# Optimization experiments

Measured on AMD Instinct MI355X. Metric: run time of the kernel, lower is better.

The kernel has to match this reference:

```python
import jax, jax.numpy as jnp
import numpy as np

B, N, IN_DIM, HIDDEN, OUT_DIM, HEADS = 4, 2048, 64, 128, 128, 4
NEG_INF = -1e9
EPS = 1e-12  # matches tf.math.l2_normalize epsilon


def setup_inputs() -> dict:
    key = jax.random.key(0)
    ks = jax.random.split(key, 13)
    d1 = HIDDEN // HEADS
    d2 = OUT_DIM // HEADS
    s = lambda k, shape, fan: jax.random.normal(k, shape, jnp.float32) * (1.0 / np.sqrt(fan))
    return {
        "x": jax.random.normal(ks[0], (B, N, IN_DIM), jnp.float32),
        "embedding": s(ks[1], (N, HIDDEN), HIDDEN),
        "Wp": s(ks[2], (IN_DIM, HIDDEN), IN_DIM),
        "bp": jnp.zeros((HIDDEN,), jnp.float32),
        "W1": s(ks[3], (HIDDEN, HIDDEN), HIDDEN),
        "a1_src": s(ks[4], (HEADS, d1), d1),
        "a1_dst": s(ks[5], (HEADS, d1), d1),
        "b1": jnp.zeros((HIDDEN,), jnp.float32),
        "W2": s(ks[6], (HIDDEN, OUT_DIM), HIDDEN),
        "a2_src": s(ks[7], (HEADS, d2), d2),
        "a2_dst": s(ks[8], (HEADS, d2), d2),
        "b2": jnp.zeros((OUT_DIM,), jnp.float32),
    }


def _gat(h, mask, W, a_src, a_dst, b, heads):
    # h: [B,N,F_in], mask: [N,N] bool (adj > 0.5), W: [F_in, heads*d]
    Bn, Nn, _ = h.shape
    d = W.shape[1] // heads
    hh = (h @ W).reshape(Bn, Nn, heads, d)                 # [B,N,H,D]
    s_src = jnp.einsum('bnhd,hd->bnh', hh, a_src)          # score of source node j
    s_dst = jnp.einsum('bnhd,hd->bnh', hh, a_dst)          # score of target node i
    # e[b,i,j,h]: raw attention logit for edge j -> i
    e = jax.nn.leaky_relu(s_dst[:, :, None, :] + s_src[:, None, :, :], 0.2)
    e = jnp.where(mask[None, :, :, None], e, NEG_INF)
    alpha = jax.nn.softmax(e, axis=2)                      # softmax over neighbors j
    out = jnp.einsum('bijh,bjhd->bihd', alpha, hh)         # aggregate messages
    return out.reshape(Bn, Nn, heads * d) + b


def reference(x, embedding, Wp, bp, W1, a1_src, a1_dst, b1, W2, a2_src, a2_dst, b2):
    # AdaptiveAdjacency: cosine similarity of learned node embeddings
    ne = embedding * jax.lax.rsqrt(jnp.sum(embedding * embedding, -1, keepdims=True) + EPS)
    adj = ne @ ne.T                                        # [N,N]
    mask = adj > 0.5                                       # dynamic edge set (diag always True)
    h = x @ Wp + bp                                        # Dense projection
    h = jax.nn.gelu(_gat(h, mask, W1, a1_src, a1_dst, b1, HEADS), approximate=False)
    return _gat(h, mask, W2, a2_src, a2_dst, b2, HEADS)
```

## Files before the change

### kernel.cpp

```cpp
#include <hip/hip_runtime.h>
#include <hip/hip_bf16.h>

using u64 = unsigned long long;

constexpr int Bb    = 4;
constexpr int Nn    = 2048;
constexpr int INDIM = 64;
constexpr int HID   = 128;
constexpr int NW    = Nn / 64;
constexpr int NT    = 16;
constexpr int NTRI  = NT * (NT + 1) / 2;

struct AdjS {
    float As[32][132];
    float Bs[32][132];
    float nA[128];
    float nB[128];
    unsigned char mb [128][16];
    unsigned char mbT[128][16];
};

__global__ __launch_bounds__(256) void k_adjproj(
        const float* __restrict__ emb, u64* __restrict__ maskw,
        const float* __restrict__ x,   const float* __restrict__ Wp,
        const float* __restrict__ bp,  const float* __restrict__ W1,
        const float* __restrict__ a1s, const float* __restrict__ a1d,
        float* __restrict__ hh1, float* __restrict__ s1s, float* __restrict__ s1d) {
    __shared__ __align__(16) unsigned char smem[sizeof(AdjS)];
    const int t = threadIdx.x;

    if (blockIdx.x < NTRI) {
        AdjS& S = *reinterpret_cast<AdjS*>(smem);
        int b = blockIdx.x, ti = 0, cum = 0;
        while (cum + (NT - ti) <= b) { cum += NT - ti; ++ti; }
        const int tj = ti + (b - cum);
        const bool diag = (ti == tj);
        const int i0 = ti * 128, j0 = tj * 128;

        const int tx = t & 15, ty = t >> 4;
        const int sr = t >> 1, sh = (t & 1) * 16;

        float acc[8][8];
        #pragma unroll
        for (int a = 0; a < 8; ++a)
            #pragma unroll
            for (int c = 0; c < 8; ++c) acc[a][c] = 0.f;

        float sqa = 0.f, sqb = 0.f;

        for (int kc = 0; kc < HID; kc += 32) {
            const float* gA = emb + (size_t)(i0 + sr) * HID + kc + sh;
            const float* gB = emb + (size_t)(j0 + sr) * HID + kc + sh;
            #pragma unroll
            for (int e = 0; e < 16; e += 4) {
                const float4 va = *reinterpret_cast<const float4*>(gA + e);
                const float4 vb = *reinterpret_cast<const float4*>(gB + e);
                S.As[sh + e + 0][sr] = va.x; S.As[sh + e + 1][sr] = va.y;
                S.As[sh + e + 2][sr] = va.z; S.As[sh + e + 3][sr] = va.w;
                sqa += va.x * va.x + va.y * va.y + va.z * va.z + va.w * va.w;
                S.Bs[sh + e + 0][sr] = vb.x; S.Bs[sh + e + 1][sr] = vb.y;
                S.Bs[sh + e + 2][sr] = vb.z; S.Bs[sh + e + 3][sr] = vb.w;
                sqb += vb.x * vb.x + vb.y * vb.y + vb.z * vb.z + vb.w * vb.w;
            }
            __syncthreads();
            #pragma unroll 4
            for (int k = 0; k < 32; ++k) {
                float a[8], c[8];
                *reinterpret_cast<float4*>(&a[0]) = *reinterpret_cast<const float4*>(&S.As[k][ty * 8]);
                *reinterpret_cast<float4*>(&a[4]) = *reinterpret_cast<const float4*>(&S.As[k][ty * 8 + 4]);
                *reinterpret_cast<float4*>(&c[0]) = *reinterpret_cast<const float4*>(&S.Bs[k][tx * 8]);
                *reinterpret_cast<float4*>(&c[4]) = *reinterpret_cast<const float4*>(&S.Bs[k][tx * 8 + 4]);
                #pragma unroll
                for (int ii = 0; ii < 8; ++ii)
                    #pragma unroll
                    for (int jj = 0; jj < 8; ++jj)
                        acc[ii][jj] += a[ii] * c[jj];
            }
            __syncthreads();
        }

        {
            const float ta = sqa + __shfl_xor(sqa, 1, 64);
            if ((t & 1) == 0) S.nA[sr] = rsqrtf(ta + 1e-12f);
            const float tb = sqb + __shfl_xor(sqb, 1, 64);
            if ((t & 1) == 0) S.nB[sr] = rsqrtf(tb + 1e-12f);
        }
        __syncthreads();

        float rsi[8], rsj[8];
        #pragma unroll
        for (int e = 0; e < 8; ++e) { rsi[e] = S.nA[ty * 8 + e]; rsj[e] = S.nB[tx * 8 + e]; }

        bool bit[8][8];
        #pragma unroll
        for (int e = 0; e < 8; ++e)
            #pragma unroll
            for (int jj = 0; jj < 8; ++jj)
                bit[e][jj] = (acc[e][jj] * rsi[e] * rsj[jj] > 0.5f);

        #pragma unroll
        for (int e = 0; e < 8; ++e) {
            unsigned byte = 0;
            #pragma unroll
            for (int jj = 0; jj < 8; ++jj) if (bit[e][jj]) byte |= (1u << jj);
            S.mb[ty * 8 + e][tx] = (unsigned char)byte;
        }
        #pragma unroll
        for (int jj = 0; jj < 8; ++jj) {
            unsigned byte = 0;
            #pragma unroll
            for (int e = 0; e < 8; ++e) if (bit[e][jj]) byte |= (1u << e);
            S.mbT[tx * 8 + jj][ty] = (unsigned char)byte;
        }
        __syncthreads();

        if (t < 128) {
            const u64* p = reinterpret_cast<const u64*>(S.mb[t]);
            maskw[(size_t)(i0 + t) * NW + 2 * tj]     = p[0];
            maskw[(size_t)(i0 + t) * NW + 2 * tj + 1] = p[1];
        } else if (!diag) {
            const int c = t - 128;
            const u64* p = reinterpret_cast<const u64*>(S.mbT[c]);
            maskw[(size_t)(j0 + c) * NW + 2 * ti]     = p[0];
            maskw[(size_t)(j0 + c) * NW + 2 * ti + 1] = p[1];
        }
    } else {
        float (*hl)[128] = reinterpret_cast<float(*)[128]>(smem);
        const int h  = t >> 7;
        const int c  = t & 127;
        const int r0 = (blockIdx.x - NTRI) * 16 + h * 8;

        float acc[8];
        const float bias = bp[c];
        #pragma unroll
        for (int r = 0; r < 8; ++r) acc[r] = bias;
        #pragma unroll 4
        for (int k = 0; k < INDIM; ++k) {
            const float wp = Wp[k * HID + c];
            #pragma unroll
            for (int r = 0; r < 8; ++r)
                acc[r] += x[(size_t)(r0 + r) * INDIM + k] * wp;
        }
        #pragma unroll
        for (int r = 0; r < 8; ++r) hl[h * 8 + r][c] = acc[r];
        __syncthreads();

        float a2[8];
        #pragma unroll
        for (int r = 0; r < 8; ++r) a2[r] = 0.f;
        #pragma unroll 4
        for (int k = 0; k < HID; ++k) {
            const float w = W1[k * HID + c];
            #pragma unroll
            for (int r = 0; r < 8; ++r)
                a2[r] += hl[h * 8 + r][k] * w;
        }
        const float as = a1s[c], ad = a1d[c];
        #pragma unroll
        for (int r = 0; r < 8; ++r) {
            hh1[(size_t)(r0 + r) * HID + c] = a2[r];
            float vs = a2[r] * as;
            float vd = a2[r] * ad;
            #pragma unroll
            for (int m = 1; m < 32; m <<= 1) {
                vs += __shfl_xor(vs, m, 32);
                vd += __shfl_xor(vd, m, 32);
            }
            if ((c & 31) == 0) {
                s1s[(size_t)(r0 + r) * 4 + (c >> 5)] = vs;
                s1d[(size_t)(r0 + r) * 4 + (c >> 5)] = vd;
            }
        }
    }
}

__global__ __launch_bounds__(128) void k_gathid2(
        const float* __restrict__ hh1,
        const float* __restrict__ s1s, const float* __restrict__ s1d,
        const u64* __restrict__ maskw, const float* __restrict__ b1v,
        const float* __restrict__ W2,
        const float* __restrict__ a2s, const float* __restrict__ a2d,
        float* __restrict__ hh2,
        float* __restrict__ s2s, float* __restrict__ s2d) {
    const int r0   = blockIdx.x * 8;
    const int bb   = r0 >> 11;
    const int t    = threadIdx.x;
    const int wv   = t >> 6;
    const int lane = t & 63;
    const int h0   = lane >> 5, h1 = 2 + h0;
    __shared__ float gl[8][128];

    for (int rr = 0; rr < 4; ++rr) {
        const int r   = wv * 4 + rr;
        const int row = r0 + r, i = row & (Nn - 1);
        const u64* mrow = maskw + (size_t)i * NW;
        const u64 myw = (lane < NW) ? mrow[lane] : 0ULL;
        u64 nz = __ballot(myw != 0ULL);
        const float sd0 = s1d[(size_t)row * 4 + h0];
        const float sd1 = s1d[(size_t)row * 4 + h1];
        float m0 = -INFINITY, l0 = 0.f, a0 = 0.f;
        float m1 = -INFINITY, l1 = 0.f, a1 = 0.f;
        while (nz) {
            const int w = __builtin_ctzll(nz); nz &= nz - 1;
            u64 word = __shfl(myw, w, 64);
            while (word) {
                const int bit = __builtin_ctzll(word); word &= word - 1;
                const int jr = (bb << 11) + (w << 6) + bit;
                float e0 = sd0 + s1s[(size_t)jr * 4 + h0];
                e0 = e0 > 0.f ? e0 : 0.2f * e0;
                float e1 = sd1 + s1s[(size_t)jr * 4 + h1];
                e1 = e1 > 0.f ? e1 : 0.2f * e1;
                const float v0 = hh1[(size_t)jr * HID + lane];
                const float v1 = hh1[(size_t)jr * HID + 64 + lane];
                float nm = fmaxf(m0, e0);
                float sc = __expf(m0 - nm);
                float p  = __expf(e0 - nm);
                l0 = l0 * sc + p; a0 = a0 * sc + p * v0; m0 = nm;
                nm = fmaxf(m1, e1);
                sc = __expf(m1 - nm);
                p  = __expf(e1 - nm);
                l1 = l1 * sc + p; a1 = a1 * sc + p * v1; m1 = nm;
            }
        }
        float o0 = (l0 > 0.f ? a0 / l0 : 0.f) + b1v[lane];
        float o1 = (l1 > 0.f ? a1 / l1 : 0.f) + b1v[64 + lane];
        o0 = 0.5f * o0 * (1.f + erff(o0 * 0.70710678118654752f));
        o1 = 0.5f * o1 * (1.f + erff(o1 * 0.70710678118654752f));
        gl[r][lane]      = o0;
        gl[r][64 + lane] = o1;
    }
    __syncthreads();

    const int c = t;
    float acc[8];
    #pragma unroll
    for (int r = 0; r < 8; ++r) acc[r] = 0.f;
    #pragma unroll 4
    for (int k = 0; k < HID; ++k) {
        const float w = W2[k * HID + c];
        #pragma unroll
        for (int r = 0; r < 8; ++r)
            acc[r] += gl[r][k] * w;
    }
    const float as = a2s[c], ad = a2d[c];
    #pragma unroll
    for (int r = 0; r < 8; ++r) {
        hh2[(size_t)(r0 + r) * HID + c] = acc[r];
        float vs = acc[r] * as;
        float vd = acc[r] * ad;
        #pragma unroll
        for (int m = 1; m < 32; m <<= 1) {
            vs += __shfl_xor(vs, m, 32);
            vd += __shfl_xor(vd, m, 32);
        }
        if ((c & 31) == 0) {
            s2s[(size_t)(r0 + r) * 4 + (c >> 5)] = vs;
            s2d[(size_t)(r0 + r) * 4 + (c >> 5)] = vd;
        }
    }
}

__global__ __launch_bounds__(256) void k_gat(const float* __restrict__ hh,
                                             const float* __restrict__ ssrc,
                                             const float* __restrict__ sdst,
                                             const u64* __restrict__ maskw,
                                             const float* __restrict__ bias,
                                             float* __restrict__ out) {
    const int row  = blockIdx.x * 4 + (threadIdx.x >> 6);
    const int i    = row & (Nn - 1);
    const int b    = row >> 11;
    const int lane = threadIdx.x & 63;
    const int h0   = lane >> 5;
    const int h1   = 2 + h0;
    const float sd0 = sdst[(size_t)row * 4 + h0];
    const float sd1 = sdst[(size_t)row * 4 + h1];
    const u64* mrow = maskw + (size_t)i * NW;

    const u64 myw = (lane < NW) ? mrow[lane] : 0ULL;
    u64 nz = __ballot(myw != 0ULL);

    float m0 = -INFINITY, l0 = 0.f, a0 = 0.f;
    float m1 = -INFINITY, l1 = 0.f, a1 = 0.f;

    while (nz) {
        const int w = __builtin_ctzll(nz); nz &= nz - 1;
        u64 word = __shfl(myw, w, 64);
        while (word) {
            const int bit = __builtin_ctzll(word); word &= word - 1;
            const int jr = (b << 11) + (w << 6) + bit;
            float e0 = sd0 + ssrc[(size_t)jr * 4 + h0];
            e0 = e0 > 0.f ? e0 : 0.2f * e0;
            float e1 = sd1 + ssrc[(size_t)jr * 4 + h1];
            e1 = e1 > 0.f ? e1 : 0.2f * e1;
            const float v0 = hh[(size_t)jr * HID + lane];
            const float v1 = hh[(size_t)jr * HID + 64 + lane];
            float nm = fmaxf(m0, e0);
            float sc = __expf(m0 - nm);
            float p  = __expf(e0 - nm);
            l0 = l0 * sc + p; a0 = a0 * sc + p * v0; m0 = nm;
            nm = fmaxf(m1, e1);
            sc = __expf(m1 - nm);
            p  = __expf(e1 - nm);
            l1 = l1 * sc + p; a1 = a1 * sc + p * v1; m1 = nm;
        }
    }

    out[(size_t)row * HID + lane]      = (l0 > 0.f ? a0 / l0 : 0.f) + bias[lane];
    out[(size_t)row * HID + 64 + lane] = (l1 > 0.f ? a1 / l1 : 0.f) + bias[64 + lane];
}

extern "C" void kernel_launch(void* const* d_in, const int* in_sizes, int n_in,
                              void* d_out, int out_size, void* d_ws, size_t ws_size,
                              hipStream_t stream) {
    const float* x   = (const float*)d_in[0];
    const float* emb = (const float*)d_in[1];
    const float* Wp  = (const float*)d_in[2];
    const float* bp  = (const float*)d_in[3];
    const float* W1  = (const float*)d_in[4];
    const float* a1s = (const float*)d_in[5];
    const float* a1d = (const float*)d_in[6];
    const float* b1  = (const float*)d_in[7];
    const float* W2  = (const float*)d_in[8];
    const float* a2s = (const float*)d_in[9];
    const float* a2d = (const float*)d_in[10];
    const float* b2  = (const float*)d_in[11];

    char* ws = (char*)d_ws;
    u64*  maskw = (u64*)ws;   ws += (size_t)Nn * NW * 8;
    float* hh1  = (float*)ws; ws += (size_t)Bb * Nn * HID * 4;
    float* hh2  = (float*)ws; ws += (size_t)Bb * Nn * HID * 4;
    float* s1s  = (float*)ws; ws += (size_t)Bb * Nn * 4 * 4;
    float* s1d  = (float*)ws; ws += (size_t)Bb * Nn * 4 * 4;
    float* s2s  = (float*)ws; ws += (size_t)Bb * Nn * 4 * 4;
    float* s2d  = (float*)ws; ws += (size_t)Bb * Nn * 4 * 4;

    k_adjproj<<<NTRI + 512, 256, 0, stream>>>(emb, maskw, x, Wp, bp, W1, a1s, a1d,
                                              hh1, s1s, s1d);
    k_gathid2<<<Bb * Nn / 8, 128, 0, stream>>>(hh1, s1s, s1d, maskw, b1,
                                               W2, a2s, a2d, hh2, s2s, s2d);
    k_gat<<<Bb * Nn / 4, 256, 0, stream>>>(hh2, s2s, s2d, maskw, b2, (float*)d_out);
}
```

Before: 49.91 us.

## Fuse layer-2 GAT aggregation into the hidden/projection kernel with on-demand recompute

Merges the layer-2 projection kernel and the final GAT kernel into one launch. Projected features and scores for the block's own 8 rows stay in shared memory. Any neighbor outside the block has its layer-1 aggregation, GELU and W2 projection recomputed inline by the wave. This removes one launch and the hh2/s2 round-trip through global memory. The cost is heavy redundant work whenever the adjacency has many off-block edges, so the gain depends on the mask being very sparse (mostly diagonal).

Measured after the change: 47.54 us. 1.05x faster.

```diff
diff --git a/kernel.cpp b/kernel.cpp
--- a/kernel.cpp
+++ b/kernel.cpp
@@ -174,21 +174,24 @@
     }
 }
 
-__global__ __launch_bounds__(128) void k_gathid2(
+__global__ __launch_bounds__(128) void k_layer2(
         const float* __restrict__ hh1,
         const float* __restrict__ s1s, const float* __restrict__ s1d,
         const u64* __restrict__ maskw, const float* __restrict__ b1v,
         const float* __restrict__ W2,
         const float* __restrict__ a2s, const float* __restrict__ a2d,
-        float* __restrict__ hh2,
-        float* __restrict__ s2s, float* __restrict__ s2d) {
-    const int r0   = blockIdx.x * 8;
-    const int bb   = r0 >> 11;
-    const int t    = threadIdx.x;
-    const int wv   = t >> 6;
-    const int lane = t & 63;
-    const int h0   = lane >> 5, h1 = 2 + h0;
+        const float* __restrict__ b2v, float* __restrict__ out) {
+    const int r0    = blockIdx.x * 8;
+    const int bb    = r0 >> 11;
+    const int iBase = r0 & (Nn - 1);
+    const int t     = threadIdx.x;
+    const int wv    = t >> 6;
+    const int lane  = t & 63;
+    const int h0    = lane >> 5, h1 = 2 + h0;
     __shared__ float gl[8][128];
+    __shared__ float h2l[8][128];
+    __shared__ float s2sl[8][4];
+    __shared__ float s2dl[8][4];
 
     for (int rr = 0; rr < 4; ++rr) {
         const int r   = wv * 4 + rr;
@@ -231,82 +234,130 @@
     }
     __syncthreads();
 
-    const int c = t;
-    float acc[8];
-    #pragma unroll
-    for (int r = 0; r < 8; ++r) acc[r] = 0.f;
-    #pragma unroll 4
-    for (int k = 0; k < HID; ++k) {
-        const float w = W2[k * HID + c];
-        #pragma unroll
-        for (int r = 0; r < 8; ++r)
-            acc[r] += gl[r][k] * w;
+    {
+        const int c = t;
+        float acc[8];
+        #pragma unroll
+        for (int r = 0; r < 8; ++r) acc[r] = 0.f;
+        #pragma unroll 4
+        for (int k = 0; k < HID; ++k) {
+            const float w = W2[k * HID + c];
+            #pragma unroll
+            for (int r = 0; r < 8; ++r)
+                acc[r] += gl[r][k] * w;
+        }
+        const float as = a2s[c], ad = a2d[c];
+        #pragma unroll
+        for (int r = 0; r < 8; ++r) {
+            h2l[r][c] = acc[r];
+            float vs = acc[r] * as;
+            float vd = acc[r] * ad;
+            #pragma unroll
+            for (int m = 1; m < 32; m <<= 1) {
+                vs += __shfl_xor(vs, m, 32);
+                vd += __shfl_xor(vd, m, 32);
+            }
+            if ((c & 31) == 0) {
+                s2sl[r][c >> 5] = vs;
+                s2dl[r][c >> 5] = vd;
+            }
+        }
     }
-    const float as = a2s[c], ad = a2d[c];
-    #pragma unroll
-    for (int r = 0; r < 8; ++r) {
-        hh2[(size_t)(r0 + r) * HID + c] = acc[r];
-        float vs = acc[r] * as;
-        float vd = acc[r] * ad;
-        #pragma unroll
-        for (int m = 1; m < 32; m <<= 1) {
-            vs += __shfl_xor(vs, m, 32);
-            vd += __shfl_xor(vd, m, 32);
-        }
-        if ((c & 31) == 0) {
-            s2s[(size_t)(r0 + r) * 4 + (c >> 5)] = vs;
-            s2d[(size_t)(r0 + r) * 4 + (c >> 5)] = vd;
-        }
+    __syncthreads();
+
+    for (int rr = 0; rr < 4; ++rr) {
+        const int r   = wv * 4 + rr;
+        const int row = r0 + r, i = row & (Nn - 1);
+        const u64* mrow = maskw + (size_t)i * NW;
+        const u64 myw = (lane < NW) ? mrow[lane] : 0ULL;
+        u64 nz = __ballot(myw != 0ULL);
+        const float sd0 = s2dl[r][h0];
+        const float sd1 = s2dl[r][h1];
+        float m0 = -INFINITY, l0 = 0.f, a0 = 0.f;
+        float m1 = -INFINITY, l1 = 0.f, a1 = 0.f;
+        while (nz) {
+            const int w = __builtin_ctzll(nz); nz &= nz - 1;
+            u64 word = __shfl(myw, w, 64);
+            while (word) {
+                const int bit = __builtin_ctzll(word); word &= word - 1;
+                const int j = (w << 6) + bit;
+                float vs0, vs1, v0, v1;
+                const unsigned lj = (unsigned)(j - iBase);
+                if (lj < 8u) {
+                    vs0 = s2sl[lj][h0]; vs1 = s2sl[lj][h1];
+                    v0  = h2l[lj][lane]; v1 = h2l[lj][64 + lane];
+                } else {
+                    const int jr = (bb << 11) + j;
+                    const u64* mrj = maskw + (size_t)j * NW;
+                    const u64 myj = (lane < NW) ? mrj[lane] : 0ULL;
+                    u64 nzj = __ballot(myj != 0ULL);
+                    const float sdj0 = s1d[(size_t)jr * 4 + h0];
+                    const float sdj1 = s1d[(size_t)jr * 4 + h1];
+                    float fm0 = -INFINITY, fl0 = 0.f, fa0 = 0.f;
+                    float fm1 = -INFINITY, fl1 = 0.f, fa1 = 0.f;
+                    while (nzj) {
+                        const int w2 = __builtin_ctzll(nzj); nzj &= nzj - 1;
+                        u64 wd = __shfl(myj, w2, 64);
+                        while (wd) {
+                            const int b2i = __builtin_ctzll(wd); wd &= wd - 1;
+                            const int k2 = (bb << 11) + (w2 << 6) + b2i;
+                            float e0 = sdj0 + s1s[(size_t)k2 * 4 + h0];
+                            e0 = e0 > 0.f ? e0 : 0.2f * e0;
+                            float e1 = sdj1 + s1s[(size_t)k2 * 4 + h1];
+                            e1 = e1 > 0.f ? e1 : 0.2f * e1;
+                            const float fv0 = hh1[(size_t)k2 * HID + lane];
+                            const float fv1 = hh1[(size_t)k2 * HID + 64 + lane];
+                            float nm = fmaxf(fm0, e0);
+                            float sc = __expf(fm0 - nm);
+                            float p  = __expf(e0 - nm);
+                            fl0 = fl0 * sc + p; fa0 = fa0 * sc + p * fv0; fm0 = nm;
+                            nm = fmaxf(fm1, e1);
+                            sc = __expf(fm1 - nm);
+                            p  = __expf(e1 - nm);
+                            fl1 = fl1 * sc + p; fa1 = fa1 * sc + p * fv1; fm1 = nm;
+                        }
+                    }
+                    float g0 = (fl0 > 0.f ? fa0 / fl0 : 0.f) + b1v[lane];
+                    float g1 = (fl1 > 0.f ? fa1 / fl1 : 0.f) + b1v[64 + lane];
+                    g0 = 0.5f * g0 * (1.f + erff(g0 * 0.70710678118654752f));
+                    g1 = 0.5f * g1 * (1.f + erff(g1 * 0.70710678118654752f));
+                    float val0 = 0.f, val1 = 0.f;
+                    for (int k = 0; k < 64; ++k) {
+                        const float gk = __shfl(g0, k, 64);
+                        val0 += gk * W2[k * HID + lane];
+                        val1 += gk * W2[k * HID + 64 + lane];
+                    }
+                    for (int k = 0; k < 64; ++k) {
+                        const float gk = __shfl(g1, k, 64);
+                        val0 += gk * W2[(64 + k) * HID + lane];
+                        val1 += gk * W2[(64 + k) * HID + 64 + lane];
+                    }
+                    float t0 = val0 * a2s[lane];
+                    float t1 = val1 * a2s[64 + lane];
+                    #pragma unroll
+                    for (int m = 1; m < 32; m <<= 1) {
+                        t0 += __shfl_xor(t0, m, 32);
+                        t1 += __shfl_xor(t1, m, 32);
+                    }
+                    vs0 = t0; vs1 = t1; v0 = val0; v1 = val1;
+                }
+                float e0 = sd0 + vs0;
+                e0 = e0 > 0.f ? e0 : 0.2f * e0;
+                float e1 = sd1 + vs1;
+                e1 = e1 > 0.f ? e1 : 0.2f * e1;
+                float nm = fmaxf(m0, e0);
+                float sc = __expf(m0 - nm);
+                float p  = __expf(e0 - nm);
+                l0 = l0 * sc + p; a0 = a0 * sc + p * v0; m0 = nm;
+                nm = fmaxf(m1, e1);
+                sc = __expf(m1 - nm);
+                p  = __expf(e1 - nm);
+                l1 = l1 * sc + p; a1 = a1 * sc + p * v1; m1 = nm;
+            }
+        }
+        out[(size_t)row * HID + lane]      = (l0 > 0.f ? a0 / l0 : 0.f) + b2v[lane];
+        out[(size_t)row * HID + 64 + lane] = (l1 > 0.f ? a1 / l1 : 0.f) + b2v[64 + lane];
     }
-}
-
-__global__ __launch_bounds__(256) void k_gat(const float* __restrict__ hh,
-                                             const float* __restrict__ ssrc,
-                                             const float* __restrict__ sdst,
-                                             const u64* __restrict__ maskw,
-                                             const float* __restrict__ bias,
-                                             float* __restrict__ out) {
-    const int row  = blockIdx.x * 4 + (threadIdx.x >> 6);
-    const int i    = row & (Nn - 1);
-    const int b    = row >> 11;
-    const int lane = threadIdx.x & 63;
-    const int h0   = lane >> 5;
-    const int h1   = 2 + h0;
-    const float sd0 = sdst[(size_t)row * 4 + h0];
-    const float sd1 = sdst[(size_t)row * 4 + h1];
-    const u64* mrow = maskw + (size_t)i * NW;
-
-    const u64 myw = (lane < NW) ? mrow[lane] : 0ULL;
-    u64 nz = __ballot(myw != 0ULL);
-
-    float m0 = -INFINITY, l0 = 0.f, a0 = 0.f;
-    float m1 = -INFINITY, l1 = 0.f, a1 = 0.f;
-
-    while (nz) {
-        const int w = __builtin_ctzll(nz); nz &= nz - 1;
-        u64 word = __shfl(myw, w, 64);
-        while (word) {
-            const int bit = __builtin_ctzll(word); word &= word - 1;
-            const int jr = (b << 11) + (w << 6) + bit;
-            float e0 = sd0 + ssrc[(size_t)jr * 4 + h0];
-            e0 = e0 > 0.f ? e0 : 0.2f * e0;
-            float e1 = sd1 + ssrc[(size_t)jr * 4 + h1];
-            e1 = e1 > 0.f ? e1 : 0.2f * e1;
-            const float v0 = hh[(size_t)jr * HID + lane];
-            const float v1 = hh[(size_t)jr * HID + 64 + lane];
-            float nm = fmaxf(m0, e0);
-            float sc = __expf(m0 - nm);
-            float p  = __expf(e0 - nm);
-            l0 = l0 * sc + p; a0 = a0 * sc + p * v0; m0 = nm;
-            nm = fmaxf(m1, e1);
-            sc = __expf(m1 - nm);
-            p  = __expf(e1 - nm);
-            l1 = l1 * sc + p; a1 = a1 * sc + p * v1; m1 = nm;
-        }
-    }
-
-    out[(size_t)row * HID + lane]      = (l0 > 0.f ? a0 / l0 : 0.f) + bias[lane];
-    out[(size_t)row * HID + 64 + lane] = (l1 > 0.f ? a1 / l1 : 0.f) + bias[64 + lane];
 }
 
 extern "C" void kernel_launch(void* const* d_in, const int* in_sizes, int n_in,
@@ -328,15 +379,11 @@
     char* ws = (char*)d_ws;
     u64*  maskw = (u64*)ws;   ws += (size_t)Nn * NW * 8;
     float* hh1  = (float*)ws; ws += (size_t)Bb * Nn * HID * 4;
-    float* hh2  = (float*)ws; ws += (size_t)Bb * Nn * HID * 4;
     float* s1s  = (float*)ws; ws += (size_t)Bb * Nn * 4 * 4;
     float* s1d  = (float*)ws; ws += (size_t)Bb * Nn * 4 * 4;
-    float* s2s  = (float*)ws; ws += (size_t)Bb * Nn * 4 * 4;
-    float* s2d  = (float*)ws; ws += (size_t)Bb * Nn * 4 * 4;
 
     k_adjproj<<<NTRI + 512, 256, 0, stream>>>(emb, maskw, x, Wp, bp, W1, a1s, a1d,
                                               hh1, s1s, s1d);
-    k_gathid2<<<Bb * Nn / 8, 128, 0, stream>>>(hh1, s1s, s1d, maskw, b1,
-                                               W2, a2s, a2d, hh2, s2s, s2d);
-    k_gat<<<Bb * Nn / 4, 256, 0, stream>>>(hh2, s2s, s2d, maskw, b2, (float*)d_out);
+    k_layer2<<<Bb * Nn / 8, 128, 0, stream>>>(hh1, s1s, s1d, maskw, b1,
+                                              W2, a2s, a2d, b2, (float*)d_out);
 }
```
